# Optimization experiments

Hardware: AMD Instinct MI355X
Metric: run time of the kernel (lower is better)

The kernel has to match this reference:

```python
import jax, jax.numpy as jnp
import numpy as np

N_NODES = 200000
N_EDGES = 6400000


def setup_inputs() -> dict:
    key = jax.random.key(0)
    ks = jax.random.split(key, 8)
    feat = jax.random.normal(ks[0], (N_NODES, 26), dtype=jnp.float32)
    src = jax.random.randint(ks[1], (N_EDGES,), 0, N_NODES, dtype=jnp.int32)
    dst = jax.random.randint(ks[2], (N_EDGES,), 0, N_NODES, dtype=jnp.int32)
    # Glorot-ish init for linear weights (scale by fan-in)
    W1_self = jax.random.normal(ks[3], (26, 40), dtype=jnp.float32) / np.sqrt(26.0)
    W1_neigh = jax.random.normal(ks[4], (26, 40), dtype=jnp.float32) / np.sqrt(26.0)
    b1 = jnp.zeros((40,), dtype=jnp.float32)
    W2_self = jax.random.normal(ks[5], (40, 24), dtype=jnp.float32) / np.sqrt(40.0)
    W2_neigh = jax.random.normal(ks[6], (40, 24), dtype=jnp.float32) / np.sqrt(40.0)
    b2 = jnp.zeros((24,), dtype=jnp.float32)
    return {"feat": feat, "src": src, "dst": dst,
            "W1_self": W1_self, "W1_neigh": W1_neigh, "b1": b1,
            "W2_self": W2_self, "W2_neigh": W2_neigh, "b2": b2}


def _sage_mean(x, src, dst, deg_inv, W_self, W_neigh, b):
    # DGL SAGEConv('mean'): fc_self(h) + fc_neigh(mean over in-neighbors) + bias
    n = x.shape[0]
    agg = jax.ops.segment_sum(x[src], dst, num_segments=n)  # [N, F]
    mean = agg * deg_inv[:, None]
    return x @ W_self + mean @ W_neigh + b


def reference(feat, src, dst, W1_self, W1_neigh, b1, W2_self, W2_neigh, b2):
    n = feat.shape[0]
    deg = jax.ops.segment_sum(jnp.ones_like(src, dtype=feat.dtype), dst, num_segments=n)
    deg_inv = jnp.where(deg > 0, 1.0 / jnp.maximum(deg, 1.0), 0.0)  # zero-degree -> 0 (DGL mean semantics)
    h = _sage_mean(feat, src, dst, deg_inv, W1_self, W1_neigh, b1)
    h = jax.nn.relu(h)
    # dropout(p=0.5) omitted: eval-mode determinism for kernel baseline
    h = _sage_mean(h, src, dst, deg_inv, W2_self, W2_neigh, b2)
    return jax.nn.log_softmax(h, axis=1)
```

## Files before the change

### kernel.cpp

```cpp
#include <hip/hip_runtime.h>
#include <math.h>


typedef long long ll;
typedef unsigned int u32;
typedef unsigned short u16;
typedef unsigned char u8;

__device__ inline u16 f2bf(float f) {
    u32 u = __builtin_bit_cast(u32, f);
    u32 r = (u + 0x7FFFu + ((u >> 16) & 1u)) >> 16;
    return (u16)r;
}
__device__ inline float bf2f(u16 h) {
    u32 u = ((u32)h) << 16;
    return __builtin_bit_cast(float, u);
}
__device__ inline u32 packbf2(float a, float b) {
    return (u32)f2bf(a) | ((u32)f2bf(b) << 16);
}

#define BSHIFT 9
#define BNODES 512
#define BCHUNK 8192
#define BCAP 22528
#define QSCALE 24.0f
#define QS2 16.0f


__global__ void __launch_bounds__(512) binf_kernel(
        const int* __restrict__ src, const int* __restrict__ dst,
        int* __restrict__ bcur, u32* __restrict__ ebuf, int n_edges, int nb, int nchunks,
        const float* __restrict__ feat, u8* __restrict__ featq, int n_nodes) {
    int t = threadIdx.x;
    if ((int)blockIdx.x >= nchunks) {
        int n = ((int)blockIdx.x - nchunks) * 512 + t;
        if (n < n_nodes) {
            const float* fr = feat + (ll)n * 26;
            float vals[26];
#pragma unroll
            for (int j = 0; j < 13; j++) {
                float2 p = *reinterpret_cast<const float2*>(fr + 2 * j);
                vals[2 * j] = p.x; vals[2 * j + 1] = p.y;
            }
            u32 w[8];
#pragma unroll
            for (int j = 0; j < 8; j++) {
                u32 wj = 0;
#pragma unroll
                for (int kk = 0; kk < 4; kk++) {
                    int c = 4 * j + kk;
                    u32 code = 128u;
                    if (c < 26) {
                        float x = vals[c] * QSCALE + 128.0f;
                        x = fminf(fmaxf(x, 0.0f), 255.0f);
                        code = (u32)(int)rintf(x);
                    }
                    wj |= code << (kk * 8);
                }
                w[j] = wj;
            }
            uint4* dp = reinterpret_cast<uint4*>(featq + (ll)n * 32);
            dp[0] = make_uint4(w[0], w[1], w[2], w[3]);
            dp[1] = make_uint4(w[4], w[5], w[6], w[7]);
        }
        return;
    }
    __shared__ int cnt[512];
    __shared__ int sc[512];
    __shared__ int loff[512];
    __shared__ int gbase[512];
    __shared__ u32 stage[BCHUNK];
    int base = blockIdx.x * BCHUNK;
    cnt[t] = 0;
    __syncthreads();
    int dv[BCHUNK / 512];
#pragma unroll
    for (int j = 0; j < BCHUNK / 512; j++) {
        int i = base + t + j * 512;
        dv[j] = (i < n_edges) ? dst[i] : -1;
        if (dv[j] >= 0) atomicAdd(&cnt[dv[j] >> BSHIFT], 1);
    }
    __syncthreads();
    int v = cnt[t];
    sc[t] = v;
    __syncthreads();
    for (int off = 1; off < 512; off <<= 1) {
        int tv = (t >= off) ? sc[t - off] : 0;
        __syncthreads();
        sc[t] += tv;
        __syncthreads();
    }
    int excl = sc[t] - v;
    loff[t] = excl;
    if (t < nb && v) gbase[t] = atomicAdd(&bcur[t], v);
    __syncthreads();
    cnt[t] = excl;
    __syncthreads();
#pragma unroll
    for (int j = 0; j < BCHUNK / 512; j++) {
        int i = base + t + j * 512;
        if (dv[j] >= 0) {
            int d = dv[j];
            int b = d >> BSHIFT;
            u32 u = ((u32)(d & (BNODES - 1)) << 18) | (u32)src[i];
            int p = atomicAdd(&cnt[b], 1);
            stage[p] = u;
        }
    }
    __syncthreads();
    int total = min(n_edges - base, BCHUNK);
    for (int i = t; i < total; i += 512) {
        int lo = 0, hi = nb - 1;
        while (lo < hi) { int mid = (lo + hi + 1) >> 1; if (i >= loff[mid]) lo = mid; else hi = mid - 1; }
        int pos = gbase[lo] + (i - loff[lo]);
        if (pos < BCAP) ebuf[(ll)lo * BCAP + pos] = stage[i];
    }
}


__global__ void __launch_bounds__(512) place3_kernel(
        const u32* __restrict__ ebuf, const int* __restrict__ bcur,
        int* __restrict__ csr, int* __restrict__ degi, int* __restrict__ endoff, int n_nodes) {
    __shared__ int cnt[512];
    __shared__ int sc[512];
    __shared__ int cur[512];
    int t = threadIdx.x;
    int b = blockIdx.x;
    ll base = (ll)b * BCAP;
    int ne = min(bcur[b], BCAP);
    const u32* ep = ebuf + base;
    cnt[t] = 0;
    __syncthreads();
    for (int i = t; i < ne; i += 512) {
        atomicAdd(&cnt[ep[i] >> 18], 1);
    }
    __syncthreads();
    int v = cnt[t];
    sc[t] = v;
    __syncthreads();
    for (int off = 1; off < 512; off <<= 1) {
        int tv = (t >= off) ? sc[t - off] : 0;
        __syncthreads();
        sc[t] += tv;
        __syncthreads();
    }
    int excl = sc[t] - v;
    cur[t] = excl;
    int node0 = b << BSHIFT;
    if (node0 + t < n_nodes) {
        degi[node0 + t] = v;
        endoff[node0 + t] = (int)base + excl + v;
    }
    __syncthreads();
    for (int i = t; i < ne; i += 512) {
        u32 u = ep[i];
        int dl = (int)(u >> 18);
        int p = atomicAdd(&cur[dl], 1);
        csr[base + p] = (int)(u & 0x3FFFFu);
    }
}


template<int FIN>
__global__ void __launch_bounds__(256) gatherq_kernel(
        const u8* __restrict__ table, const int* __restrict__ csr,
        const int* __restrict__ endoff, const int* __restrict__ degi,
        u16* __restrict__ meanb, float* __restrict__ outp, int n_nodes) {
    int g = (blockIdx.x * 256 + threadIdx.x) >> 5;
    if (g >= n_nodes) return;
    int lane = threadIdx.x & 31;
    int slot = lane >> 2;
    int q = lane & 3;
    int end = endoff[g];
    int dg = degi[g];
    int start = end - dg;
    float acc[8];
#pragma unroll
    for (int j = 0; j < 8; j++) acc[j] = 0.0f;
    int k = start;
    for (; k + 32 <= end; k += 32) {
        int myid = csr[k + lane];
#pragma unroll
        for (int it = 0; it < 4; it++) {
            int nidx = (it << 3) + slot;
            int s = __shfl(myid, nidx, 32);
            uint2 v = *reinterpret_cast<const uint2*>(table + ((ll)s << 5) + (q << 3));
            acc[0] += (float)(v.x & 0xFFu);         acc[1] += (float)((v.x >> 8) & 0xFFu);
            acc[2] += (float)((v.x >> 16) & 0xFFu); acc[3] += (float)(v.x >> 24);
            acc[4] += (float)(v.y & 0xFFu);         acc[5] += (float)((v.y >> 8) & 0xFFu);
            acc[6] += (float)((v.y >> 16) & 0xFFu); acc[7] += (float)(v.y >> 24);
        }
    }
    if (k < end) {
        int cnt = end - k;
        int myid = (lane < cnt) ? csr[k + lane] : 0;
#pragma unroll
        for (int it = 0; it < 4; it++) {
            if ((it << 3) >= cnt) break;
            int nidx = (it << 3) + slot;
            int s = __shfl(myid, nidx, 32);
            if (nidx < cnt) {
                uint2 v = *reinterpret_cast<const uint2*>(table + ((ll)s << 5) + (q << 3));
                acc[0] += (float)(v.x & 0xFFu);         acc[1] += (float)((v.x >> 8) & 0xFFu);
                acc[2] += (float)((v.x >> 16) & 0xFFu); acc[3] += (float)(v.x >> 24);
                acc[4] += (float)(v.y & 0xFFu);         acc[5] += (float)((v.y >> 8) & 0xFFu);
                acc[6] += (float)((v.y >> 16) & 0xFFu); acc[7] += (float)(v.y >> 24);
            }
        }
    }
#pragma unroll
    for (int m = 4; m <= 16; m <<= 1) {
#pragma unroll
        for (int j = 0; j < 8; j++) acc[j] += __shfl_xor(acc[j], m, 32);
    }
    float dinv = dg > 0 ? 1.0f / (float)dg : 0.0f;
    if (FIN == 0) {
        if (lane < 4) {
            float scl = dg > 0 ? dinv * (1.0f / QSCALE) : 0.0f;
            float off = dg > 0 ? (128.0f / QSCALE) : 0.0f;
            u32 w0 = packbf2(acc[0] * scl - off, acc[1] * scl - off);
            u32 w1 = packbf2(acc[2] * scl - off, acc[3] * scl - off);
            u32 w2 = packbf2(acc[4] * scl - off, acc[5] * scl - off);
            u32 w3 = packbf2(acc[6] * scl - off, acc[7] * scl - off);
            *reinterpret_cast<uint4*>(meanb + ((ll)g << 5) + (q << 3)) = make_uint4(w0, w1, w2, w3);
        }
    } else {
        if (lane < 4) {
            float scl = dg > 0 ? dinv * (1.0f / QS2) : 0.0f;
            float off = dg > 0 ? (128.0f / QS2) : 0.0f;
            float v[8];
            float m = -3.4e38f;
            if (q < 3) {
                float4 o0 = *reinterpret_cast<const float4*>(outp + (ll)g * 24 + (q << 3));
                float4 o1 = *reinterpret_cast<const float4*>(outp + (ll)g * 24 + (q << 3) + 4);
                v[0] = o0.x + acc[0] * scl - off; v[1] = o0.y + acc[1] * scl - off;
                v[2] = o0.z + acc[2] * scl - off; v[3] = o0.w + acc[3] * scl - off;
                v[4] = o1.x + acc[4] * scl - off; v[5] = o1.y + acc[5] * scl - off;
                v[6] = o1.z + acc[6] * scl - off; v[7] = o1.w + acc[7] * scl - off;
#pragma unroll
                for (int j = 0; j < 8; j++) m = fmaxf(m, v[j]);
            }
#pragma unroll
            for (int mk = 1; mk <= 2; mk <<= 1) m = fmaxf(m, __shfl_xor(m, mk, 32));
            float es = 0.0f;
            if (q < 3) {
#pragma unroll
                for (int j = 0; j < 8; j++) es += expf(v[j] - m);
            }
#pragma unroll
            for (int mk = 1; mk <= 2; mk <<= 1) es += __shfl_xor(es, mk, 32);
            if (q < 3) {
                float l = m + logf(es);
                float4 r0 = make_float4(v[0] - l, v[1] - l, v[2] - l, v[3] - l);
                float4 r1 = make_float4(v[4] - l, v[5] - l, v[6] - l, v[7] - l);
                *reinterpret_cast<float4*>(outp + (ll)g * 24 + (q << 3)) = r0;
                *reinterpret_cast<float4*>(outp + (ll)g * 24 + (q << 3) + 4) = r1;
            }
        }
    }
}


__global__ void __launch_bounds__(256) node_mlp_kernel(
        const float* __restrict__ feat, const u16* __restrict__ meanb,
        const float* __restrict__ W1s, const float* __restrict__ W1n, const float* __restrict__ b1,
        const float* __restrict__ W2s, const float* __restrict__ W2n, const float* __restrict__ b2,
        float* __restrict__ outp, u8* __restrict__ t2q, int n_nodes) {
    __shared__ float sW1s[26 * 40];
    __shared__ float sW1n[26 * 40];
    __shared__ float sW2s[40 * 24];
    __shared__ float sW2n[40 * 24];
    __shared__ float sb1[40];
    __shared__ float sb2[24];
    int t = threadIdx.x;
    for (int i = t; i < 26 * 40; i += 256) { sW1s[i] = W1s[i]; sW1n[i] = W1n[i]; }
    for (int i = t; i < 40 * 24; i += 256) { sW2s[i] = W2s[i]; sW2n[i] = W2n[i]; }
    if (t < 40) sb1[t] = b1[t];
    if (t < 24) sb2[t] = b2[t];
    __syncthreads();

    int n = blockIdx.x * 256 + t;
    if (n >= n_nodes) return;

    float h[40];
#pragma unroll
    for (int j = 0; j < 40; j++) h[j] = sb1[j];

    const float* fr = feat + (ll)n * 26;
    const u16* br = meanb + ((ll)n << 5);
#pragma unroll
    for (int k = 0; k < 26; k++) {
        float f = fr[k];
        float a = bf2f(br[k]);
#pragma unroll
        for (int j = 0; j < 40; j++) h[j] += f * sW1s[k * 40 + j] + a * sW1n[k * 40 + j];
    }
#pragma unroll
    for (int j = 0; j < 40; j++) h[j] = h[j] > 0.0f ? h[j] : 0.0f;

    float o[24], tt[24];
#pragma unroll
    for (int j = 0; j < 24; j++) { o[j] = sb2[j]; tt[j] = 0.0f; }
#pragma unroll
    for (int k = 0; k < 40; k++) {
        float hv = h[k];
#pragma unroll
        for (int j = 0; j < 24; j++) {
            o[j]  += hv * sW2s[k * 24 + j];
            tt[j] += hv * sW2n[k * 24 + j];
        }
    }
    float* op = outp + (ll)n * 24;
#pragma unroll
    for (int j = 0; j < 24; j++) op[j] = o[j];
    u32 w[8];
#pragma unroll
    for (int j = 0; j < 6; j++) {
        u32 wj = 0;
#pragma unroll
        for (int kk = 0; kk < 4; kk++) {
            float x = tt[4 * j + kk] * QS2 + 128.0f;
            x = fminf(fmaxf(x, 0.0f), 255.0f);
            wj |= ((u32)(int)rintf(x)) << (kk * 8);
        }
        w[j] = wj;
    }
    w[6] = 0x80808080u;
    w[7] = 0x80808080u;
    uint4* dp = reinterpret_cast<uint4*>(t2q + ((ll)n << 5));
    dp[0] = make_uint4(w[0], w[1], w[2], w[3]);
    dp[1] = make_uint4(w[4], w[5], w[6], w[7]);
}


__global__ void hist_kernel(const int* __restrict__ dst, int* __restrict__ degi, int n_edges) {
    int i = blockIdx.x * blockDim.x + threadIdx.x;
    int base = i * 4;
    if (base + 3 < n_edges) {
        int4 d = *reinterpret_cast<const int4*>(dst + base);
        atomicAdd(&degi[d.x], 1);
        atomicAdd(&degi[d.y], 1);
        atomicAdd(&degi[d.z], 1);
        atomicAdd(&degi[d.w], 1);
    } else {
        for (int e = base; e < n_edges; e++) atomicAdd(&degi[dst[e]], 1);
    }
}

__global__ void __launch_bounds__(256) scan1_kernel(const int* __restrict__ in, int* __restrict__ out,
                                                    int* __restrict__ bsums, int n) {
    __shared__ int lds[256];
    int t = threadIdx.x;
    int base = blockIdx.x * 2048 + t * 8;
    int v[8];
    int s = 0;
#pragma unroll
    for (int i = 0; i < 8; i++) { v[i] = (base + i < n) ? in[base + i] : 0; s += v[i]; }
    lds[t] = s;
    __syncthreads();
    for (int off = 1; off < 256; off <<= 1) {
        int tv = (t >= off) ? lds[t - off] : 0;
        __syncthreads();
        lds[t] += tv;
        __syncthreads();
    }
    int excl = lds[t] - s;
    if (t == 255) bsums[blockIdx.x] = lds[255];
    int run = excl;
#pragma unroll
    for (int i = 0; i < 8; i++) {
        if (base + i < n) out[base + i] = run;
        run += v[i];
    }
}

__global__ void __launch_bounds__(256) scan2_kernel(int* __restrict__ bsums, int nb) {
    __shared__ int lds[256];
    int t = threadIdx.x;
    int v = (t < nb) ? bsums[t] : 0;
    lds[t] = v;
    __syncthreads();
    for (int off = 1; off < 256; off <<= 1) {
        int tv = (t >= off) ? lds[t - off] : 0;
        __syncthreads();
        lds[t] += tv;
        __syncthreads();
    }
    if (t < nb) bsums[t] = lds[t] - v;
}

__global__ void scan3_kernel(int* __restrict__ out, const int* __restrict__ bsums, int n) {
    int i = blockIdx.x * blockDim.x + threadIdx.x;
    if (i < n) out[i] += bsums[i >> 11];
}

__global__ void place_kernel(const int* __restrict__ src, const int* __restrict__ dst,
                             int* __restrict__ cursor, int* __restrict__ csr, int n_edges) {
    int e = blockIdx.x * blockDim.x + threadIdx.x;
    if (e < n_edges) {
        int d = dst[e];
        int pos = atomicAdd(&cursor[d], 1);
        csr[pos] = src[e];
    }
}

__global__ void __launch_bounds__(256) gather_mean26_kernel(
        const float* __restrict__ feat, const int* __restrict__ csr,
        const int* __restrict__ endoff, const int* __restrict__ degi,
        float* __restrict__ buf, int n_nodes) {
    int g = (blockIdx.x * 256 + threadIdx.x) >> 5;
    int lane = threadIdx.x & 31;
    if (g >= n_nodes) return;
    int end = endoff[g];
    int dg = degi[g];
    int start = end - dg;
    int c = lane < 26 ? lane : 0;
    float acc = 0.0f;
    int k = start;
    while (k < end) {
        int cnt = min(end - k, 32);
        int myid = (k + lane < end) ? csr[k + lane] : 0;
#pragma unroll 4
        for (int j = 0; j < cnt; j++) {
            int s = __shfl(myid, j, 32);
            acc += feat[(ll)s * 26 + c];
        }
        k += cnt;
    }
    float dinv = dg > 0 ? 1.0f / (float)dg : 0.0f;
    if (lane < 26) buf[(ll)g * 26 + lane] = acc * dinv;
}

__global__ void __launch_bounds__(256) node_mlp_fb_kernel(
        const float* __restrict__ feat, float* buf,
        const float* __restrict__ W1s, const float* __restrict__ W1n, const float* __restrict__ b1,
        const float* __restrict__ W2s, const float* __restrict__ W2n, const float* __restrict__ b2,
        float* __restrict__ outp, int n_nodes) {
    __shared__ float sW1s[26 * 40];
    __shared__ float sW1n[26 * 40];
    __shared__ float sW2s[40 * 24];
    __shared__ float sW2n[40 * 24];
    __shared__ float sb1[40];
    __shared__ float sb2[24];
    int t = threadIdx.x;
    for (int i = t; i < 26 * 40; i += 256) { sW1s[i] = W1s[i]; sW1n[i] = W1n[i]; }
    for (int i = t; i < 40 * 24; i += 256) { sW2s[i] = W2s[i]; sW2n[i] = W2n[i]; }
    if (t < 40) sb1[t] = b1[t];
    if (t < 24) sb2[t] = b2[t];
    __syncthreads();
    int n = blockIdx.x * 256 + t;
    if (n >= n_nodes) return;
    float h[40];
#pragma unroll
    for (int j = 0; j < 40; j++) h[j] = sb1[j];
    const float* fr = feat + (ll)n * 26;
    float* br = buf + (ll)n * 26;
#pragma unroll
    for (int k = 0; k < 26; k++) {
        float f = fr[k];
        float a = br[k];
#pragma unroll
        for (int j = 0; j < 40; j++) h[j] += f * sW1s[k * 40 + j] + a * sW1n[k * 40 + j];
    }
#pragma unroll
    for (int j = 0; j < 40; j++) h[j] = h[j] > 0.0f ? h[j] : 0.0f;
    float o[24], tt[24];
#pragma unroll
    for (int j = 0; j < 24; j++) { o[j] = sb2[j]; tt[j] = 0.0f; }
#pragma unroll
    for (int k = 0; k < 40; k++) {
        float hv = h[k];
#pragma unroll
        for (int j = 0; j < 24; j++) {
            o[j]  += hv * sW2s[k * 24 + j];
            tt[j] += hv * sW2n[k * 24 + j];
        }
    }
    float* op = outp + (ll)n * 24;
#pragma unroll
    for (int j = 0; j < 24; j++) op[j] = o[j];
#pragma unroll
    for (int j = 0; j < 24; j++) br[j] = tt[j];
}

__global__ void __launch_bounds__(256) gather_fin24_kernel(
        const float* __restrict__ buf, const int* __restrict__ csr,
        const int* __restrict__ endoff, const int* __restrict__ degi,
        float* __restrict__ outp, int n_nodes) {
    int g = (blockIdx.x * 256 + threadIdx.x) >> 5;
    int lane = threadIdx.x & 31;
    if (g >= n_nodes) return;
    int end = endoff[g];
    int dg = degi[g];
    int start = end - dg;
    int c = lane < 24 ? lane : 0;
    float acc = 0.0f;
    int k = start;
    while (k < end) {
        int cnt = min(end - k, 32);
        int myid = (k + lane < end) ? csr[k + lane] : 0;
#pragma unroll 4
        for (int j = 0; j < cnt; j++) {
            int s = __shfl(myid, j, 32);
            acc += buf[(ll)s * 26 + c];
        }
        k += cnt;
    }
    float dinv = dg > 0 ? 1.0f / (float)dg : 0.0f;
    float v = (lane < 24) ? outp[(ll)g * 24 + lane] + acc * dinv : -INFINITY;
    float m = v;
#pragma unroll
    for (int mask = 16; mask >= 1; mask >>= 1) m = fmaxf(m, __shfl_xor(m, mask, 32));
    float ex = (lane < 24) ? expf(v - m) : 0.0f;
    float ssum = ex;
#pragma unroll
    for (int mask = 16; mask >= 1; mask >>= 1) ssum += __shfl_xor(ssum, mask, 32);
    if (lane < 24) outp[(ll)g * 24 + lane] = v - m - logf(ssum);
}


extern "C" void kernel_launch(void* const* d_in, const int* in_sizes, int n_in,
                              void* d_out, int out_size, void* d_ws, size_t ws_size,
                              hipStream_t stream) {
    const float* feat = (const float*)d_in[0];
    const int*   src  = (const int*)d_in[1];
    const int*   dst  = (const int*)d_in[2];
    const float* W1s  = (const float*)d_in[3];
    const float* W1n  = (const float*)d_in[4];
    const float* b1   = (const float*)d_in[5];
    const float* W2s  = (const float*)d_in[6];
    const float* W2n  = (const float*)d_in[7];
    const float* b2   = (const float*)d_in[8];

    int n_nodes = in_sizes[0] / 26;
    int n_edges = in_sizes[1];
    float* out = (float*)d_out;

    int NB = (n_nodes + BNODES - 1) >> BSHIFT;

    size_t off = 0;
    auto alloc = [&off](size_t cnt) { size_t r = off; off += (cnt + 3) & ~(size_t)3; return r; };
    size_t ebuf_cnt = (size_t)NB * BCAP;
    if (ebuf_cnt < (size_t)n_nodes * 16) ebuf_cnt = (size_t)n_nodes * 16;
    size_t o_bcur = alloc(512);
    size_t o_ebuf = alloc(ebuf_cnt);
    size_t o_csr  = alloc((size_t)NB * BCAP);
    size_t o_tab  = alloc((size_t)n_nodes * 8);
    size_t o_degi = alloc(n_nodes);
    size_t o_endo = alloc(n_nodes);
    size_t need = off * 4;

    bool fast = (NB <= 512) && (n_nodes <= (1 << 18)) && (ws_size >= need) &&
                ((ll)n_edges * 5 <= (ll)NB * BCAP * 4);

    if (fast) {
        int* base    = (int*)d_ws;
        int* bcur    = base + o_bcur;
        u32* ebuf    = (u32*)(base + o_ebuf);
        int* csr     = base + o_csr;
        u8*  featq   = (u8*)(base + o_tab);
        u8*  t2q     = featq;
        u16* meanb   = (u16*)ebuf;
        int* degi    = base + o_degi;
        int* endoff  = base + o_endo;

        hipMemsetAsync(bcur, 0, sizeof(int) * 512, stream);

        int nchunks = (n_edges + BCHUNK - 1) / BCHUNK;
        int fqblocks = (n_nodes + 511) / 512;
        binf_kernel<<<nchunks + fqblocks, 512, 0, stream>>>(
            src, dst, bcur, ebuf, n_edges, NB, nchunks, feat, featq, n_nodes);

        place3_kernel<<<NB, 512, 0, stream>>>(ebuf, bcur, csr, degi, endoff, n_nodes);

        int gather_blocks = (n_nodes * 32 + 255) / 256;
        gatherq_kernel<0><<<gather_blocks, 256, 0, stream>>>(featq, csr, endoff, degi, meanb, nullptr, n_nodes);

        node_mlp_kernel<<<(n_nodes + 255) / 256, 256, 0, stream>>>(
            feat, meanb, W1s, W1n, b1, W2s, W2n, b2, out, t2q, n_nodes);

        gatherq_kernel<1><<<gather_blocks, 256, 0, stream>>>(t2q, csr, endoff, degi, nullptr, out, n_nodes);
    } else {
        int* degi  = (int*)d_ws;
        int* offs  = degi + n_nodes;
        int* bsums = offs + n_nodes;
        int* csr   = bsums + 256;
        float* buf = (float*)(csr + n_edges);

        hipMemsetAsync(degi, 0, sizeof(int) * (size_t)n_nodes, stream);
        {
            int work = (n_edges + 3) / 4;
            hist_kernel<<<(work + 255) / 256, 256, 0, stream>>>(dst, degi, n_edges);
        }
        int scan_blocks = (n_nodes + 2047) / 2048;
        scan1_kernel<<<scan_blocks, 256, 0, stream>>>(degi, offs, bsums, n_nodes);
        scan2_kernel<<<1, 256, 0, stream>>>(bsums, scan_blocks);
        scan3_kernel<<<(n_nodes + 255) / 256, 256, 0, stream>>>(offs, bsums, n_nodes);

        place_kernel<<<(n_edges + 255) / 256, 256, 0, stream>>>(src, dst, offs, csr, n_edges);

        int gather_blocks = (n_nodes * 32 + 255) / 256;
        gather_mean26_kernel<<<gather_blocks, 256, 0, stream>>>(feat, csr, offs, degi, buf, n_nodes);

        node_mlp_fb_kernel<<<(n_nodes + 255) / 256, 256, 0, stream>>>(
            feat, buf, W1s, W1n, b1, W2s, W2n, b2, out, n_nodes);

        gather_fin24_kernel<<<gather_blocks, 256, 0, stream>>>(buf, csr, offs, degi, out, n_nodes);
    }
}
```

Before: 327.0 us.

## Store bucket ids in staging, coalesce feature loads via LDS, vectorize MLP IO

In the binning kernel, each staged edge now also records its bucket id in a shared u16 array, so the scatter loop no longer runs a binary search over bucket offsets. The edge chunk size shrinks to make room for that array in shared memory. In the node MLP kernel, the block's feature rows are copied into shared memory with coalesced float4 loads, each thread reads its bf16 mean row as four uint4 loads, and the output row is written as float4. The trade-off is more shared memory per block, which may lower occupancy, and a larger number of binning blocks.

```diff
diff --git a/kernel.cpp b/kernel.cpp
--- a/kernel.cpp
+++ b/kernel.cpp
@@ -22,7 +22,7 @@
 
 #define BSHIFT 9
 #define BNODES 512
-#define BCHUNK 8192
+#define BCHUNK 6144
 #define BCAP 22528
 #define QSCALE 24.0f
 #define QS2 16.0f
@@ -71,6 +71,7 @@
     __shared__ int loff[512];
     __shared__ int gbase[512];
     __shared__ u32 stage[BCHUNK];
+    __shared__ u16 stageb[BCHUNK];
     int base = blockIdx.x * BCHUNK;
     cnt[t] = 0;
     __syncthreads();
@@ -106,15 +107,15 @@
             u32 u = ((u32)(d & (BNODES - 1)) << 18) | (u32)src[i];
             int p = atomicAdd(&cnt[b], 1);
             stage[p] = u;
+            stageb[p] = (u16)b;
         }
     }
     __syncthreads();
     int total = min(n_edges - base, BCHUNK);
     for (int i = t; i < total; i += 512) {
-        int lo = 0, hi = nb - 1;
-        while (lo < hi) { int mid = (lo + hi + 1) >> 1; if (i >= loff[mid]) lo = mid; else hi = mid - 1; }
-        int pos = gbase[lo] + (i - loff[lo]);
-        if (pos < BCAP) ebuf[(ll)lo * BCAP + pos] = stage[i];
+        int b = (int)stageb[i];
+        int pos = gbase[b] + (i - loff[b]);
+        if (pos < BCAP) ebuf[(ll)b * BCAP + pos] = stage[i];
     }
 }
 
@@ -273,26 +274,45 @@
     __shared__ float sW2n[40 * 24];
     __shared__ float sb1[40];
     __shared__ float sb2[24];
+    __shared__ float sfeat[256 * 26];
     int t = threadIdx.x;
     for (int i = t; i < 26 * 40; i += 256) { sW1s[i] = W1s[i]; sW1n[i] = W1n[i]; }
     for (int i = t; i < 40 * 24; i += 256) { sW2s[i] = W2s[i]; sW2n[i] = W2n[i]; }
     if (t < 40) sb1[t] = b1[t];
     if (t < 24) sb2[t] = b2[t];
-    __syncthreads();
-
-    int n = blockIdx.x * 256 + t;
-    if (n >= n_nodes) return;
+
+    int node0 = blockIdx.x * 256;
+    int nloc = min(256, n_nodes - node0);
+    int nfl = nloc * 26;
+    {
+        const float4* gsrc = reinterpret_cast<const float4*>(feat + (ll)node0 * 26);
+        float4* ldst = reinterpret_cast<float4*>(sfeat);
+        int n4 = nfl >> 2;
+        for (int i = t; i < n4; i += 256) ldst[i] = gsrc[i];
+        for (int i = (n4 << 2) + t; i < nfl; i += 256) sfeat[i] = feat[(ll)node0 * 26 + i];
+    }
+    __syncthreads();
+
+    if (t >= nloc) return;
+    int n = node0 + t;
 
     float h[40];
 #pragma unroll
     for (int j = 0; j < 40; j++) h[j] = sb1[j];
 
-    const float* fr = feat + (ll)n * 26;
-    const u16* br = meanb + ((ll)n << 5);
+    const float* fr = sfeat + t * 26;
+    uint4 mrow[4];
+    {
+        const uint4* mp = reinterpret_cast<const uint4*>(meanb + ((ll)n << 5));
+        mrow[0] = mp[0]; mrow[1] = mp[1]; mrow[2] = mp[2]; mrow[3] = mp[3];
+    }
+    const u32* mw = reinterpret_cast<const u32*>(mrow);
 #pragma unroll
     for (int k = 0; k < 26; k++) {
         float f = fr[k];
-        float a = bf2f(br[k]);
+        u32 w = mw[k >> 1];
+        float a = (k & 1) ? __builtin_bit_cast(float, w & 0xFFFF0000u)
+                          : __builtin_bit_cast(float, w << 16);
 #pragma unroll
         for (int j = 0; j < 40; j++) h[j] += f * sW1s[k * 40 + j] + a * sW1n[k * 40 + j];
     }
@@ -311,9 +331,10 @@
             tt[j] += hv * sW2n[k * 24 + j];
         }
     }
-    float* op = outp + (ll)n * 24;
-#pragma unroll
-    for (int j = 0; j < 24; j++) op[j] = o[j];
+    float4* op4 = reinterpret_cast<float4*>(outp + (ll)n * 24);
+#pragma unroll
+    for (int z = 0; z < 6; z++)
+        op4[z] = make_float4(o[4 * z], o[4 * z + 1], o[4 * z + 2], o[4 * z + 3]);
     u32 w[8];
 #pragma unroll
     for (int j = 0; j < 6; j++) {
```

New measurement: 313.6 us. 1.04x faster.
